# Optimization experiments

Hardware: AMD Instinct MI355X
Metric: run time of the kernel (lower is better)

The kernel has to match this reference:

```python
import jax, jax.numpy as jnp
import numpy as np

N_ATOM_TYPES = 100
EMBED_DIM = 32
HIDDEN_DIM = 256
B, W, D = 16, 256, 64


def setup_inputs() -> dict:
    key = jax.random.key(0)
    ks = jax.random.split(key, 16)
    inp = {
        "atom1_idx": jax.random.randint(ks[0], (B, W, D), 0, N_ATOM_TYPES),
        "atom2_idx": jax.random.randint(ks[1], (B, W, D), 0, N_ATOM_TYPES),
        "distances": jax.random.uniform(ks[2], (B, W, D), jnp.float32) * 20.0,
        "mask": jax.random.bernoulli(ks[3], 0.9, (B, W, D)),
        # parameters
        "atom_embed": jax.random.normal(ks[4], (N_ATOM_TYPES + 1, EMBED_DIM), jnp.float32) * 0.02,
        "w_in": jax.random.normal(ks[5], (2 * EMBED_DIM + 1, HIDDEN_DIM), jnp.float32) * 0.05,
        "b_in": jnp.zeros((HIDDEN_DIM,), jnp.float32),
        "w_a1": jax.random.normal(ks[6], (HIDDEN_DIM, HIDDEN_DIM // 4), jnp.float32) * 0.05,
        "b_a1": jnp.zeros((HIDDEN_DIM // 4,), jnp.float32),
        "w_a2": jax.random.normal(ks[7], (HIDDEN_DIM // 4, 1), jnp.float32) * 0.05,
        "b_a2": jnp.zeros((1,), jnp.float32),
        "w_v1": jax.random.normal(ks[8], (HIDDEN_DIM, HIDDEN_DIM), jnp.float32) * 0.05,
        "b_v1": jnp.zeros((HIDDEN_DIM,), jnp.float32),
        "w_v2": jax.random.normal(ks[9], (HIDDEN_DIM, HIDDEN_DIM), jnp.float32) * 0.05,
        "b_v2": jnp.zeros((HIDDEN_DIM,), jnp.float32),
        "fallback": jnp.zeros((HIDDEN_DIM,), jnp.float32),
    }
    return inp


def _gelu(x):
    return jax.nn.gelu(x, approximate=False)  # torch default GELU is exact erf form


def reference(atom1_idx, atom2_idx, distances, mask,
              atom_embed, w_in, b_in, w_a1, b_a1, w_a2, b_a2,
              w_v1, b_v1, w_v2, b_v2, fallback):
    # zero padding row (padding_idx = n_atom_types); also kills its grad like torch
    pad = atom_embed.shape[0] - 1
    table = atom_embed * (jnp.arange(atom_embed.shape[0]) != pad)[:, None]
    e1 = table[atom1_idx]                     # [B,W,D,E]
    e2 = table[atom2_idx]                     # [B,W,D,E]
    d = distances * mask.astype(distances.dtype)
    combined = jnp.concatenate([e1, e2, d[..., None]], axis=-1)   # [B,W,D,2E+1]
    hidden = _gelu(combined @ w_in + b_in)    # [B,W,D,H] (dropout = identity in eval)
    scores = (_gelu(hidden @ w_a1 + b_a1) @ w_a2 + b_a2)[..., 0]  # [B,W,D]
    scores = jnp.where(mask, scores, jnp.float32(-10000.0))
    attn = jax.nn.softmax(scores, axis=-1)    # [B,W,D]
    values = _gelu(hidden @ w_v1 + b_v1) @ w_v2 + b_v2            # [B,W,D,H]
    out = jnp.sum(values * attn[..., None], axis=2)               # [B,W,H]
    any_valid = jnp.any(mask, axis=2)
    return jnp.where(any_valid[..., None], out, fallback)
```

## Files before the change

### kernel.cpp

```cpp
#include <hip/hip_runtime.h>
#include <math.h>

#define BW 4096
#define DD 64
#define HH 256

typedef __bf16 bf16x8 __attribute__((ext_vector_type(8)));
typedef float  f32x4  __attribute__((ext_vector_type(4)));
typedef unsigned short u16x8 __attribute__((ext_vector_type(8)));

#define WIN_OFF 0
#define WA1_OFF 16384
#define WV1_OFF 32768
#define WV2_OFF 98304

__device__ __forceinline__ unsigned short to_bf16u(float f) {
    union { __bf16 b; unsigned short u; } cv;
    cv.b = (__bf16)f;
    return cv.u;
}

__device__ __forceinline__ float gelu_fast(float x) {
    float x2 = x * x;
    float z  = x * __builtin_fmaf(-0.10294344f, x2, -2.3022082f);
    float e  = __builtin_amdgcn_exp2f(z);
    return x * __builtin_amdgcn_rcpf(1.0f + e);
}

__device__ __forceinline__ f32x4 mfma16(bf16x8 a, bf16x8 b, f32x4 c) {
    return __builtin_amdgcn_mfma_f32_16x16x32_bf16(a, b, c, 0, 0, 0);
}

__global__ void pack_weights(const float* __restrict__ w_in,
                             const float* __restrict__ w_a1,
                             const float* __restrict__ w_v1,
                             const float* __restrict__ w_v2,
                             unsigned short* __restrict__ ws) {
    int t = blockIdx.x * 256 + threadIdx.x;
    if (t >= 20480) return;
    int lane = t & 63;
    int g = lane >> 4, li = lane & 15;
    u16x8 v;
    if (t < 2048) {
        int fr = t >> 6;
        int kin = fr >> 4, ht = fr & 15;
        #pragma unroll
        for (int j = 0; j < 8; ++j) {
            int k = kin * 32 + 8 * g + j;
            v[j] = to_bf16u(w_in[(size_t)k * 256 + 16 * ht + li]);
        }
        *(u16x8*)(ws + WIN_OFF + (size_t)t * 8) = v;
    } else if (t < 4096) {
        int c = t - 2048;
        int fr = c >> 6;
        int kt = fr >> 2, ct = fr & 3;
        #pragma unroll
        for (int j = 0; j < 8; ++j) {
            int k = kt * 32 + 16 * (j >> 2) + 4 * g + (j & 3);
            v[j] = to_bf16u(w_a1[(size_t)k * 64 + ct * 16 + li]);
        }
        *(u16x8*)(ws + WA1_OFF + (size_t)c * 8) = v;
    } else if (t < 12288) {
        int c = t - 4096;
        int fr = c >> 6;
        int kt = fr >> 4, ct = fr & 15;
        #pragma unroll
        for (int j = 0; j < 8; ++j) {
            int k = kt * 32 + 16 * (j >> 2) + 4 * g + (j & 3);
            v[j] = to_bf16u(w_v1[(size_t)k * 256 + ct * 16 + li]);
        }
        *(u16x8*)(ws + WV1_OFF + (size_t)c * 8) = v;
    } else {
        int c = t - 12288;
        int fr = c >> 6;
        int kt = fr >> 4, ct = fr & 15;
        #pragma unroll
        for (int j = 0; j < 8; ++j) {
            int k = kt * 32 + 8 * g + j;
            v[j] = to_bf16u(w_v2[(size_t)k * 256 + ct * 16 + li]);
        }
        *(u16x8*)(ws + WV2_OFF + (size_t)c * 8) = v;
    }
}

__global__ __launch_bounds__(256, 4)
void dist_attn_kernel(const int*   __restrict__ a1,
                      const int*   __restrict__ a2,
                      const float* __restrict__ dist,
                      const int*   __restrict__ mask,
                      const float* __restrict__ table,
                      const float* __restrict__ w_in,
                      const float* __restrict__ b_in,
                      const float* __restrict__ b_a1,
                      const float* __restrict__ w_a2,
                      const float* __restrict__ b_a2,
                      const float* __restrict__ b_v1,
                      const float* __restrict__ b_v2,
                      const float* __restrict__ fb,
                      const unsigned short* __restrict__ ws,
                      float*       __restrict__ out) {
    __shared__ __align__(16) unsigned char sU[8192];
    __shared__ __align__(16) unsigned short hidfrag[4][8][64][8];

    unsigned short (*combfrag)[2][64][8] = (unsigned short (*)[2][64][8])sU;
    float*          scorep = (float*)sU;
    float*          attn_s = (float*)(sU + 1024);
    unsigned short* r_bf   = (unsigned short*)(sU + 2048);

    const int tid = threadIdx.x;
    const int l   = tid & 63;
    const int w   = tid >> 6;
    const int g   = l >> 4;
    const int li  = l & 15;
    const int blk = blockIdx.x;
    const long base = (long)blk * DD;

    {
        const int i1 = a1[base + 16 * w + li];
        const int i2 = a2[base + 16 * w + li];
        #pragma unroll
        for (int ks = 0; ks < 2; ++ks) {
            const int idx = ks ? i2 : i1;
            const float* srcp = table + (size_t)idx * 32 + 8 * g;
            f32x4 v0 = *(const f32x4*)srcp;
            f32x4 v1 = *(const f32x4*)(srcp + 4);
            u16x8 u;
            #pragma unroll
            for (int j = 0; j < 4; ++j) { u[j] = to_bf16u(v0[j]); u[j + 4] = to_bf16u(v1[j]); }
            *(u16x8*)&combfrag[w][ks][l][0] = u;
        }
    }
    __syncthreads();

    {
        bf16x8 cb[4][2];
        #pragma unroll
        for (int dt = 0; dt < 4; ++dt)
            #pragma unroll
            for (int ks = 0; ks < 2; ++ks)
                cb[dt][ks] = *(const bf16x8*)&combfrag[dt][ks][l][0];
        float dmv[4];
        #pragma unroll
        for (int dt = 0; dt < 4; ++dt) {
            int m = mask[base + 16 * dt + li];
            dmv[dt] = m ? dist[base + 16 * dt + li] : 0.0f;
        }
        #pragma unroll
        for (int hp = 0; hp < 2; ++hp) {
            u16x8 pend[4];
            #pragma unroll
            for (int b = 0; b < 2; ++b) {
                const int ht = 4 * w + 2 * hp + b;
                bf16x8 af0 = *(const bf16x8*)(ws + WIN_OFF + ((0 * 16 + ht) * 64 + l) * 8);
                bf16x8 af1 = *(const bf16x8*)(ws + WIN_OFF + ((1 * 16 + ht) * 64 + l) * 8);
                f32x4 w64v = *(const f32x4*)&w_in[64 * 256 + 16 * ht + 4 * g];
                f32x4 binv = *(const f32x4*)&b_in[16 * ht + 4 * g];
                #pragma unroll
                for (int dt = 0; dt < 4; ++dt) {
                    f32x4 acc = {0.f, 0.f, 0.f, 0.f};
                    acc = mfma16(af0, cb[dt][0], acc);
                    acc = mfma16(af1, cb[dt][1], acc);
                    #pragma unroll
                    for (int p = 0; p < 4; ++p) {
                        float h = gelu_fast(acc[p] + dmv[dt] * w64v[p] + binv[p]);
                        pend[dt][4 * b + p] = to_bf16u(h);
                    }
                }
            }
            #pragma unroll
            for (int dt = 0; dt < 4; ++dt)
                *(u16x8*)&hidfrag[dt][2 * w + hp][l][0] = pend[dt];
        }
    }
    __syncthreads();

    {
        const float ba1 = b_a1[16 * w + li];
        const float wa2 = w_a2[16 * w + li];
        f32x4 acc[4];
        #pragma unroll
        for (int rt = 0; rt < 4; ++rt) acc[rt] = (f32x4){0.f, 0.f, 0.f, 0.f};
        #pragma unroll
        for (int kt = 0; kt < 8; ++kt) {
            bf16x8 b = *(const bf16x8*)(ws + WA1_OFF + ((kt * 4 + w) * 64 + l) * 8);
            #pragma unroll
            for (int rt = 0; rt < 4; ++rt) {
                bf16x8 a = *(const bf16x8*)&hidfrag[rt][kt][l][0];
                acc[rt] = mfma16(a, b, acc[rt]);
            }
        }
        #pragma unroll
        for (int rt = 0; rt < 4; ++rt) {
            float s[4];
            #pragma unroll
            for (int p = 0; p < 4; ++p) s[p] = gelu_fast(acc[rt][p] + ba1) * wa2;
            #pragma unroll
            for (int off = 1; off <= 8; off <<= 1)
                #pragma unroll
                for (int p = 0; p < 4; ++p) s[p] += __shfl_xor(s[p], off, 64);
            if (li == 0) {
                f32x4 sv; sv[0] = s[0]; sv[1] = s[1]; sv[2] = s[2]; sv[3] = s[3];
                *(f32x4*)&scorep[w * 64 + 16 * rt + 4 * g] = sv;
            }
        }
    }
    __syncthreads();

    {
        const int m = mask[base + l];
        float sc = scorep[l] + scorep[64 + l] + scorep[128 + l] + scorep[192 + l] + b_a2[0];
        if (!m) sc = -10000.0f;
        float mx = sc;
        #pragma unroll
        for (int off = 32; off; off >>= 1) mx = fmaxf(mx, __shfl_xor(mx, off, 64));
        float p = __expf(sc - mx);
        float sm = p;
        #pragma unroll
        for (int off = 32; off; off >>= 1) sm += __shfl_xor(sm, off, 64);
        attn_s[w * 64 + l] = p / sm;
    }

    {
        f32x4 av[4];
        #pragma unroll
        for (int rt = 0; rt < 4; ++rt) av[rt] = *(const f32x4*)&attn_s[w * 64 + 16 * rt + 4 * g];
        #pragma unroll
        for (int half = 0; half < 2; ++half) {
            f32x4 acc3[2][4];
            #pragma unroll
            for (int c2 = 0; c2 < 2; ++c2)
                #pragma unroll
                for (int rt = 0; rt < 4; ++rt) acc3[c2][rt] = (f32x4){0.f, 0.f, 0.f, 0.f};
            #pragma unroll
            for (int kt = 0; kt < 8; ++kt) {
                bf16x8 a[4];
                #pragma unroll
                for (int rt = 0; rt < 4; ++rt) a[rt] = *(const bf16x8*)&hidfrag[rt][kt][l][0];
                #pragma unroll
                for (int c2 = 0; c2 < 2; ++c2) {
                    const int ct = 2 * half + c2;
                    bf16x8 b = *(const bf16x8*)(ws + WV1_OFF + ((kt * 16 + 4 * w + ct) * 64 + l) * 8);
                    #pragma unroll
                    for (int rt = 0; rt < 4; ++rt) acc3[c2][rt] = mfma16(a[rt], b, acc3[c2][rt]);
                }
            }
            #pragma unroll
            for (int c2 = 0; c2 < 2; ++c2) {
                const int ct = 2 * half + c2;
                const int c = 64 * w + 16 * ct + li;
                const float bv = b_v1[c];
                float val = 0.f;
                #pragma unroll
                for (int rt = 0; rt < 4; ++rt)
                    #pragma unroll
                    for (int p = 0; p < 4; ++p)
                        val += av[rt][p] * gelu_fast(acc3[c2][rt][p] + bv);
                val += __shfl_xor(val, 16, 64);
                val += __shfl_xor(val, 32, 64);
                if (g == 0) r_bf[c] = to_bf16u(val);
            }
        }
    }
    __syncthreads();

    {
        const int anyv = __any(mask[base + l] != 0);
        f32x4 acc[4];
        #pragma unroll
        for (int ct = 0; ct < 4; ++ct) acc[ct] = (f32x4){0.f, 0.f, 0.f, 0.f};
        #pragma unroll
        for (int kt = 0; kt < 8; ++kt) {
            bf16x8 a = *(const bf16x8*)&r_bf[kt * 32 + 8 * g];
            #pragma unroll
            for (int ct = 0; ct < 4; ++ct) {
                bf16x8 b = *(const bf16x8*)(ws + WV2_OFF + ((kt * 16 + 4 * w + ct) * 64 + l) * 8);
                acc[ct] = mfma16(a, b, acc[ct]);
            }
        }
        if (g == 0) {
            #pragma unroll
            for (int ct = 0; ct < 4; ++ct) {
                const int c = 16 * (4 * w + ct) + li;
                float o = acc[ct][0] + b_v2[c];
                if (!anyv) o = fb[c];
                out[(size_t)blk * HH + c] = o;
            }
        }
    }
}

extern "C" void kernel_launch(void* const* d_in, const int* in_sizes, int n_in,
                              void* d_out, int out_size, void* d_ws, size_t ws_size,
                              hipStream_t stream) {
    const int*   a1    = (const int*)  d_in[0];
    const int*   a2    = (const int*)  d_in[1];
    const float* dist  = (const float*)d_in[2];
    const int*   mask  = (const int*)  d_in[3];
    const float* table = (const float*)d_in[4];
    const float* w_in  = (const float*)d_in[5];
    const float* b_in  = (const float*)d_in[6];
    const float* w_a1  = (const float*)d_in[7];
    const float* b_a1  = (const float*)d_in[8];
    const float* w_a2  = (const float*)d_in[9];
    const float* b_a2  = (const float*)d_in[10];
    const float* w_v1  = (const float*)d_in[11];
    const float* b_v1  = (const float*)d_in[12];
    const float* w_v2  = (const float*)d_in[13];
    const float* b_v2  = (const float*)d_in[14];
    const float* fb    = (const float*)d_in[15];
    float* out = (float*)d_out;
    unsigned short* ws = (unsigned short*)d_ws;

    pack_weights<<<80, 256, 0, stream>>>(w_in, w_a1, w_v1, w_v2, ws);
    dist_attn_kernel<<<BW, 256, 0, stream>>>(a1, a2, dist, mask, table,
                                             w_in, b_in, b_a1, w_a2, b_a2,
                                             b_v1, b_v2, fb, ws, out);
}
```

Before: 102.3 us.

## Gather embeddings directly into registers and drop combfrag shared staging

Each wave now gathers the embedding rows for all four row tiles straight into MFMA operand registers instead of staging them through shared memory. This removes one __syncthreads and the LDS round-trip. The distance and bias term is folded into the accumulator init before the MFMAs. The W_a1 fragments are hoisted ahead of the MFMA loop, and the W_v1 loads are reordered, to overlap global latency. The cost is 4x redundant table gathers per block (every wave loads every row) and higher register pressure at 4 blocks per CU.

```diff
diff --git a/kernel.cpp b/kernel.cpp
--- a/kernel.cpp
+++ b/kernel.cpp
@@ -99,13 +99,10 @@
                       const float* __restrict__ fb,
                       const unsigned short* __restrict__ ws,
                       float*       __restrict__ out) {
-    __shared__ __align__(16) unsigned char sU[8192];
     __shared__ __align__(16) unsigned short hidfrag[4][8][64][8];
-
-    unsigned short (*combfrag)[2][64][8] = (unsigned short (*)[2][64][8])sU;
-    float*          scorep = (float*)sU;
-    float*          attn_s = (float*)(sU + 1024);
-    unsigned short* r_bf   = (unsigned short*)(sU + 2048);
+    __shared__ __align__(16) float scorep[256];
+    __shared__ __align__(16) float attn_s[256];
+    __shared__ __align__(16) unsigned short r_bf[256];
 
     const int tid = threadIdx.x;
     const int l   = tid & 63;
@@ -116,84 +113,81 @@
     const long base = (long)blk * DD;
 
     {
-        const int i1 = a1[base + 16 * w + li];
-        const int i2 = a2[base + 16 * w + li];
-        #pragma unroll
-        for (int ks = 0; ks < 2; ++ks) {
-            const int idx = ks ? i2 : i1;
-            const float* srcp = table + (size_t)idx * 32 + 8 * g;
-            f32x4 v0 = *(const f32x4*)srcp;
-            f32x4 v1 = *(const f32x4*)(srcp + 4);
-            u16x8 u;
-            #pragma unroll
-            for (int j = 0; j < 4; ++j) { u[j] = to_bf16u(v0[j]); u[j + 4] = to_bf16u(v1[j]); }
-            *(u16x8*)&combfrag[w][ks][l][0] = u;
-        }
-    }
-    __syncthreads();
-
-    {
         bf16x8 cb[4][2];
-        #pragma unroll
-        for (int dt = 0; dt < 4; ++dt)
-            #pragma unroll
-            for (int ks = 0; ks < 2; ++ks)
-                cb[dt][ks] = *(const bf16x8*)&combfrag[dt][ks][l][0];
-        float dmv[4];
+        float  dmv[4];
         #pragma unroll
         for (int dt = 0; dt < 4; ++dt) {
-            int m = mask[base + 16 * dt + li];
+            const int i1 = a1[base + 16 * dt + li];
+            const int i2 = a2[base + 16 * dt + li];
+            const int m  = mask[base + 16 * dt + li];
             dmv[dt] = m ? dist[base + 16 * dt + li] : 0.0f;
+            const float* s1 = table + (size_t)i1 * 32 + 8 * g;
+            const float* s2 = table + (size_t)i2 * 32 + 8 * g;
+            f32x4 v0 = *(const f32x4*)s1;
+            f32x4 v1 = *(const f32x4*)(s1 + 4);
+            f32x4 v2 = *(const f32x4*)s2;
+            f32x4 v3 = *(const f32x4*)(s2 + 4);
+            #pragma unroll
+            for (int j = 0; j < 4; ++j) {
+                cb[dt][0][j]     = (__bf16)v0[j];
+                cb[dt][0][j + 4] = (__bf16)v1[j];
+                cb[dt][1][j]     = (__bf16)v2[j];
+                cb[dt][1][j + 4] = (__bf16)v3[j];
+            }
         }
         #pragma unroll
         for (int hp = 0; hp < 2; ++hp) {
-            u16x8 pend[4];
+            bf16x8 pend[4];
             #pragma unroll
             for (int b = 0; b < 2; ++b) {
                 const int ht = 4 * w + 2 * hp + b;
-                bf16x8 af0 = *(const bf16x8*)(ws + WIN_OFF + ((0 * 16 + ht) * 64 + l) * 8);
-                bf16x8 af1 = *(const bf16x8*)(ws + WIN_OFF + ((1 * 16 + ht) * 64 + l) * 8);
+                bf16x8 af0 = *(const bf16x8*)(ws + WIN_OFF + ((size_t)(0 * 16 + ht) * 64 + l) * 8);
+                bf16x8 af1 = *(const bf16x8*)(ws + WIN_OFF + ((size_t)(1 * 16 + ht) * 64 + l) * 8);
                 f32x4 w64v = *(const f32x4*)&w_in[64 * 256 + 16 * ht + 4 * g];
                 f32x4 binv = *(const f32x4*)&b_in[16 * ht + 4 * g];
                 #pragma unroll
                 for (int dt = 0; dt < 4; ++dt) {
-                    f32x4 acc = {0.f, 0.f, 0.f, 0.f};
+                    f32x4 acc;
+                    #pragma unroll
+                    for (int p = 0; p < 4; ++p)
+                        acc[p] = __builtin_fmaf(dmv[dt], w64v[p], binv[p]);
                     acc = mfma16(af0, cb[dt][0], acc);
                     acc = mfma16(af1, cb[dt][1], acc);
                     #pragma unroll
-                    for (int p = 0; p < 4; ++p) {
-                        float h = gelu_fast(acc[p] + dmv[dt] * w64v[p] + binv[p]);
-                        pend[dt][4 * b + p] = to_bf16u(h);
-                    }
+                    for (int p = 0; p < 4; ++p)
+                        pend[dt][4 * b + p] = (__bf16)gelu_fast(acc[p]);
                 }
             }
             #pragma unroll
             for (int dt = 0; dt < 4; ++dt)
-                *(u16x8*)&hidfrag[dt][2 * w + hp][l][0] = pend[dt];
+                *(bf16x8*)&hidfrag[dt][2 * w + hp][l][0] = pend[dt];
         }
     }
     __syncthreads();
 
     {
+        bf16x8 ba[8];
+        #pragma unroll
+        for (int kt = 0; kt < 8; ++kt)
+            ba[kt] = *(const bf16x8*)(ws + WA1_OFF + ((size_t)(kt * 4 + w) * 64 + l) * 8);
+        f32x4 acc2[4];
+        #pragma unroll
+        for (int rt = 0; rt < 4; ++rt) acc2[rt] = (f32x4){0.f, 0.f, 0.f, 0.f};
+        #pragma unroll
+        for (int kt = 0; kt < 8; ++kt) {
+            #pragma unroll
+            for (int rt = 0; rt < 4; ++rt) {
+                bf16x8 a = *(const bf16x8*)&hidfrag[rt][kt][l][0];
+                acc2[rt] = mfma16(a, ba[kt], acc2[rt]);
+            }
+        }
         const float ba1 = b_a1[16 * w + li];
         const float wa2 = w_a2[16 * w + li];
-        f32x4 acc[4];
-        #pragma unroll
-        for (int rt = 0; rt < 4; ++rt) acc[rt] = (f32x4){0.f, 0.f, 0.f, 0.f};
-        #pragma unroll
-        for (int kt = 0; kt < 8; ++kt) {
-            bf16x8 b = *(const bf16x8*)(ws + WA1_OFF + ((kt * 4 + w) * 64 + l) * 8);
-            #pragma unroll
-            for (int rt = 0; rt < 4; ++rt) {
-                bf16x8 a = *(const bf16x8*)&hidfrag[rt][kt][l][0];
-                acc[rt] = mfma16(a, b, acc[rt]);
-            }
-        }
         #pragma unroll
         for (int rt = 0; rt < 4; ++rt) {
             float s[4];
             #pragma unroll
-            for (int p = 0; p < 4; ++p) s[p] = gelu_fast(acc[rt][p] + ba1) * wa2;
+            for (int p = 0; p < 4; ++p) s[p] = gelu_fast(acc2[rt][p] + ba1) * wa2;
             #pragma unroll
             for (int off = 1; off <= 8; off <<= 1)
                 #pragma unroll
@@ -233,15 +227,15 @@
                 for (int rt = 0; rt < 4; ++rt) acc3[c2][rt] = (f32x4){0.f, 0.f, 0.f, 0.f};
             #pragma unroll
             for (int kt = 0; kt < 8; ++kt) {
+                bf16x8 b0 = *(const bf16x8*)(ws + WV1_OFF + ((size_t)(kt * 16 + 4 * w + 2 * half + 0) * 64 + l) * 8);
+                bf16x8 b1 = *(const bf16x8*)(ws + WV1_OFF + ((size_t)(kt * 16 + 4 * w + 2 * half + 1) * 64 + l) * 8);
                 bf16x8 a[4];
                 #pragma unroll
                 for (int rt = 0; rt < 4; ++rt) a[rt] = *(const bf16x8*)&hidfrag[rt][kt][l][0];
                 #pragma unroll
-                for (int c2 = 0; c2 < 2; ++c2) {
-                    const int ct = 2 * half + c2;
-                    bf16x8 b = *(const bf16x8*)(ws + WV1_OFF + ((kt * 16 + 4 * w + ct) * 64 + l) * 8);
-                    #pragma unroll
-                    for (int rt = 0; rt < 4; ++rt) acc3[c2][rt] = mfma16(a[rt], b, acc3[c2][rt]);
+                for (int rt = 0; rt < 4; ++rt) {
+                    acc3[0][rt] = mfma16(a[rt], b0, acc3[0][rt]);
+                    acc3[1][rt] = mfma16(a[rt], b1, acc3[1][rt]);
                 }
             }
             #pragma unroll
@@ -273,7 +267,7 @@
             bf16x8 a = *(const bf16x8*)&r_bf[kt * 32 + 8 * g];
             #pragma unroll
             for (int ct = 0; ct < 4; ++ct) {
-                bf16x8 b = *(const bf16x8*)(ws + WV2_OFF + ((kt * 16 + 4 * w + ct) * 64 + l) * 8);
+                bf16x8 b = *(const bf16x8*)(ws + WV2_OFF + ((size_t)(kt * 16 + 4 * w + ct) * 64 + l) * 8);
                 acc[ct] = mfma16(a, b, acc[ct]);
             }
         }
```

Measured after the change: 111.2 us. 1.09x slower.
